# Optimization experiments

Hardware: AMD Instinct MI355X
Metric: run time of the kernel (lower is better)

The kernel has to match this reference:

```python
import jax, jax.numpy as jnp
import numpy as np

K = 21                     # kernel_size
LAM = 128.0                # lam
SIGMA_SPACE = 32.0
SIGMA_LUMA = 8.0
H = 512
W = 512
HO = H - K + 1             # valid conv output height (492)
WO = W - K + 1
C = (K - 1) // 2           # center offset (10)
CTR = C * K + C            # center channel index in row-major K*K patches


def _diff_patches(x):
    """x: (H, W) float. Returns (K*K-1, HO, WO): center pixel minus each
    of the other K*K-1 window taps (== the sparse 2-tap conv in torch)."""
    p = jax.lax.conv_general_dilated_patches(
        x[None, None], (K, K), (1, 1), 'VALID')[0]      # (K*K, HO, WO)
    diffs = p[CTR][None] - p                             # center - neighbor
    return jnp.delete(diffs, CTR, axis=0)                # drop all-zero center chan


def _make_w_ij(ref_hwc):
    """Bilateral affinity weights, per the torch __init__."""
    pos_x = jnp.broadcast_to(jnp.arange(W, dtype=jnp.float32)[None, :], (H, W))
    pos_y = jnp.broadcast_to(jnp.arange(H, dtype=jnp.float32)[:, None], (H, W))
    dx = _diff_patches(pos_x)
    dy = _diff_patches(pos_y)
    log_w = -(dx * dx + dy * dy) / (2.0 * SIGMA_SPACE ** 2)
    for c in range(ref_hwc.shape[-1]):                   # fixed 3 channels
        dr = _diff_patches(ref_hwc[:, :, c])
        log_w = log_w - dr * dr / (2.0 * SIGMA_LUMA ** 2)
    return jnp.exp(log_w)                                # (K*K-1, HO, WO)


def setup_inputs() -> dict:
    key = jax.random.key(0)
    k1, k2, k3 = jax.random.split(key, 3)
    output = jax.random.uniform(k1, (H, W), dtype=jnp.float32)   # logits/255
    target = jax.random.uniform(k2, (H, W), dtype=jnp.float32)   # target/255
    ref = jax.random.uniform(k3, (H, W, 3), dtype=jnp.float32) * 255.0
    w_ij = _make_w_ij(ref)
    bias = jnp.zeros((K * K - 1,), dtype=jnp.float32)   # torch conv bias (zeroed)
    return {"output": output, "target": target, "w_ij": w_ij, "bias": bias}


def reference(output, target, w_ij, bias):
    d = _diff_patches(output) + bias[:, None, None]      # (K*K-1, HO, WO)
    smooth = (H * W) * LAM * jnp.mean(w_ij * d * d)
    fidelity = jnp.mean((output - target) ** 2)
    return smooth + fidelity
```

## Files before the change

### kernel.cpp

```cpp
#include <hip/hip_runtime.h>

constexpr int Kk   = 21;
constexpr int Hh   = 512, Ww = 512;
constexpr int HO   = 492, WO = 492;
constexpr int Cc   = 10;
constexpr int CTRi = 220;
constexpr int NCH  = 440;
constexpr int ROW4 = WO / 4;
constexpr int N4S  = NCH * HO * ROW4;
constexpr int N4F  = Hh * Ww / 4;

typedef float floatx4 __attribute__((ext_vector_type(4)));

#define TPB  256
#define NB_S 1024
#define NB_F 64

__device__ __forceinline__ float block_reduce_256(float v) {
    #pragma unroll
    for (int off = 32; off; off >>= 1) v += __shfl_down(v, off, 64);
    __shared__ float smem[TPB / 64];
    const int lane = threadIdx.x & 63;
    const int wid  = threadIdx.x >> 6;
    if (lane == 0) smem[wid] = v;
    __syncthreads();
    float r = 0.f;
    if (threadIdx.x == 0) {
        #pragma unroll
        for (int k = 0; k < TPB / 64; ++k) r += smem[k];
    }
    return r;
}

__global__ __launch_bounds__(TPB) void smooth_partial_kernel(
        const float* __restrict__ outp,
        const float* __restrict__ w,
        const float* __restrict__ bias,
        float* __restrict__ partial)
{
    float acc = 0.f;
    const int stride = gridDim.x * blockDim.x;
    for (int q = blockIdx.x * blockDim.x + threadIdx.x; q < N4S; q += stride) {
        const int r  = q / ROW4;
        const int j  = (q - r * ROW4) * 4;
        const int n  = r / HO;
        const int i  = r - n * HO;
        const int kk = n + (n >= CTRi ? 1 : 0);
        const int ki = kk / Kk;
        const int kj = kk - ki * Kk;

        const floatx4 w4 = __builtin_nontemporal_load(((const floatx4*)w) + q);

        const float* crow = outp + (i + Cc) * Ww + (Cc + j);
        const float* nrow = outp + (i + ki) * Ww + (kj + j);
        const float  b    = bias[n];

        const float d0 = crow[0] - nrow[0] + b;
        const float d1 = crow[1] - nrow[1] + b;
        const float d2 = crow[2] - nrow[2] + b;
        const float d3 = crow[3] - nrow[3] + b;

        acc += w4.x * d0 * d0 + w4.y * d1 * d1 + w4.z * d2 * d2 + w4.w * d3 * d3;
    }
    const float bsum = block_reduce_256(acc);
    if (threadIdx.x == 0) partial[blockIdx.x] = bsum;
}

__global__ __launch_bounds__(TPB) void fid_partial_kernel(
        const float* __restrict__ outp,
        const float* __restrict__ targ,
        float* __restrict__ partial)
{
    float acc = 0.f;
    const int stride = gridDim.x * blockDim.x;
    for (int q = blockIdx.x * blockDim.x + threadIdx.x; q < N4F; q += stride) {
        const floatx4 a = ((const floatx4*)outp)[q];
        const floatx4 t = ((const floatx4*)targ)[q];
        const float d0 = a.x - t.x, d1 = a.y - t.y, d2 = a.z - t.z, d3 = a.w - t.w;
        acc += d0 * d0 + d1 * d1 + d2 * d2 + d3 * d3;
    }
    const float bsum = block_reduce_256(acc);
    if (threadIdx.x == 0) partial[blockIdx.x] = bsum;
}

__global__ __launch_bounds__(64) void finalize_kernel(
        const float* __restrict__ ps,
        const float* __restrict__ pf,
        float* __restrict__ out)
{
    const int t = threadIdx.x;
    float s = 0.f;
    for (int i = t; i < NB_S; i += 64) s += ps[i];
    float f = pf[t];
    #pragma unroll
    for (int off = 32; off; off >>= 1) {
        s += __shfl_down(s, off, 64);
        f += __shfl_down(f, off, 64);
    }
    if (t == 0) {
        const float SCALE_S = (float)((512.0 * 512.0 * 128.0) / (440.0 * 492.0 * 492.0));
        const float SCALE_F = 1.0f / (512.0f * 512.0f);
        out[0] = s * SCALE_S + f * SCALE_F;
    }
}

extern "C" void kernel_launch(void* const* d_in, const int* in_sizes, int n_in,
                              void* d_out, int out_size, void* d_ws, size_t ws_size,
                              hipStream_t stream) {
    const float* outp = (const float*)d_in[0];
    const float* targ = (const float*)d_in[1];
    const float* w    = (const float*)d_in[2];
    const float* bias = (const float*)d_in[3];

    float* ps = (float*)d_ws;
    float* pf = ps + NB_S;

    smooth_partial_kernel<<<NB_S, TPB, 0, stream>>>(outp, w, bias, ps);
    fid_partial_kernel<<<NB_F, TPB, 0, stream>>>(outp, targ, pf);
    finalize_kernel<<<1, 64, 0, stream>>>(ps, pf, (float*)d_out);
}
```

Baseline: 559.2 us.

## Fuse fidelity into smooth kernel with row-block and channel-split tiling

```diff
diff --git a/kernel.cpp b/kernel.cpp
--- a/kernel.cpp
+++ b/kernel.cpp
@@ -7,14 +7,20 @@
 constexpr int CTRi = 220;
 constexpr int NCH  = 440;
 constexpr int ROW4 = WO / 4;
-constexpr int N4S  = NCH * HO * ROW4;
 constexpr int N4F  = Hh * Ww / 4;
+
+constexpr int RSPLIT = HO / 2;
+constexpr int CSPLIT = 8;
+constexpr int NPB    = NCH / CSPLIT;
+constexpr int NBLK   = RSPLIT * CSPLIT;
+
+constexpr float SCALE_S  = (float)((512.0 * 512.0 * 128.0) / (440.0 * 492.0 * 492.0));
+constexpr float FID_RATIO = (float)((1.0 / (512.0 * 512.0)) /
+                                    ((512.0 * 512.0 * 128.0) / (440.0 * 492.0 * 492.0)));
 
 typedef float floatx4 __attribute__((ext_vector_type(4)));
 
-#define TPB  256
-#define NB_S 1024
-#define NB_F 64
+#define TPB 256
 
 __device__ __forceinline__ float block_reduce_256(float v) {
     #pragma unroll
@@ -32,76 +38,79 @@
     return r;
 }
 
-__global__ __launch_bounds__(TPB) void smooth_partial_kernel(
+__global__ __launch_bounds__(TPB) void main_kernel(
         const float* __restrict__ outp,
+        const float* __restrict__ targ,
         const float* __restrict__ w,
         const float* __restrict__ bias,
         float* __restrict__ partial)
 {
+    const int t = threadIdx.x;
     float acc = 0.f;
-    const int stride = gridDim.x * blockDim.x;
-    for (int q = blockIdx.x * blockDim.x + threadIdx.x; q < N4S; q += stride) {
-        const int r  = q / ROW4;
-        const int j  = (q - r * ROW4) * 4;
-        const int n  = r / HO;
-        const int i  = r - n * HO;
-        const int kk = n + (n >= CTRi ? 1 : 0);
-        const int ki = kk / Kk;
-        const int kj = kk - ki * Kk;
 
-        const floatx4 w4 = __builtin_nontemporal_load(((const floatx4*)w) + q);
+    {
+        const int fq = blockIdx.x * TPB + t;
+        if (fq < N4F) {
+            const floatx4 a  = ((const floatx4*)outp)[fq];
+            const floatx4 tg = ((const floatx4*)targ)[fq];
+            const float d0 = a.x - tg.x, d1 = a.y - tg.y,
+                        d2 = a.z - tg.z, d3 = a.w - tg.w;
+            acc = (d0 * d0 + d1 * d1 + d2 * d2 + d3 * d3) * FID_RATIO;
+        }
+    }
+
+    const int rowblk = blockIdx.x % RSPLIT;
+    const int csplit = blockIdx.x / RSPLIT;
+    const int n0     = csplit * NPB;
+
+    if (t < 2 * ROW4) {
+        const int di = (t >= ROW4) ? 1 : 0;
+        const int j4 = t - di * ROW4;
+        const int i  = rowblk * 2 + di;
+        const int j  = 4 * j4;
 
         const float* crow = outp + (i + Cc) * Ww + (Cc + j);
-        const float* nrow = outp + (i + ki) * Ww + (kj + j);
-        const float  b    = bias[n];
+        const float c0 = crow[0], c1 = crow[1], c2 = crow[2], c3 = crow[3];
 
-        const float d0 = crow[0] - nrow[0] + b;
-        const float d1 = crow[1] - nrow[1] + b;
-        const float d2 = crow[2] - nrow[2] + b;
-        const float d3 = crow[3] - nrow[3] + b;
+        const float* obase = outp + i * Ww + j;
+        const floatx4* wp  = (const floatx4*)w + ((long)(n0 * HO + i) * ROW4 + j4);
 
-        acc += w4.x * d0 * d0 + w4.y * d1 * d1 + w4.z * d2 * d2 + w4.w * d3 * d3;
+        float a0 = 0.f, a1 = 0.f, a2 = 0.f, a3 = 0.f;
+        #pragma unroll 5
+        for (int n = n0; n < n0 + NPB; ++n, wp += HO * ROW4) {
+            const int kk = n + (n >= CTRi ? 1 : 0);
+            const int ki = kk / Kk;
+            const int kj = kk - ki * Kk;
+
+            const floatx4 w4 = __builtin_nontemporal_load(wp);
+            const float   b  = bias[n];
+            const float*  nr = obase + ki * Ww + kj;
+
+            const float d0 = c0 - nr[0] + b;
+            const float d1 = c1 - nr[1] + b;
+            const float d2 = c2 - nr[2] + b;
+            const float d3 = c3 - nr[3] + b;
+
+            a0 += w4.x * d0 * d0;
+            a1 += w4.y * d1 * d1;
+            a2 += w4.z * d2 * d2;
+            a3 += w4.w * d3 * d3;
+        }
+        acc += (a0 + a1) + (a2 + a3);
     }
+
     const float bsum = block_reduce_256(acc);
-    if (threadIdx.x == 0) partial[blockIdx.x] = bsum;
+    if (t == 0) partial[blockIdx.x] = bsum;
 }
 
-__global__ __launch_bounds__(TPB) void fid_partial_kernel(
-        const float* __restrict__ outp,
-        const float* __restrict__ targ,
-        float* __restrict__ partial)
-{
-    float acc = 0.f;
-    const int stride = gridDim.x * blockDim.x;
-    for (int q = blockIdx.x * blockDim.x + threadIdx.x; q < N4F; q += stride) {
-        const floatx4 a = ((const floatx4*)outp)[q];
-        const floatx4 t = ((const floatx4*)targ)[q];
-        const float d0 = a.x - t.x, d1 = a.y - t.y, d2 = a.z - t.z, d3 = a.w - t.w;
-        acc += d0 * d0 + d1 * d1 + d2 * d2 + d3 * d3;
-    }
-    const float bsum = block_reduce_256(acc);
-    if (threadIdx.x == 0) partial[blockIdx.x] = bsum;
-}
-
-__global__ __launch_bounds__(64) void finalize_kernel(
-        const float* __restrict__ ps,
-        const float* __restrict__ pf,
+__global__ __launch_bounds__(TPB) void finalize_kernel(
+        const float* __restrict__ partial,
         float* __restrict__ out)
 {
-    const int t = threadIdx.x;
-    float s = 0.f;
-    for (int i = t; i < NB_S; i += 64) s += ps[i];
-    float f = pf[t];
-    #pragma unroll
-    for (int off = 32; off; off >>= 1) {
-        s += __shfl_down(s, off, 64);
-        f += __shfl_down(f, off, 64);
-    }
-    if (t == 0) {
-        const float SCALE_S = (float)((512.0 * 512.0 * 128.0) / (440.0 * 492.0 * 492.0));
-        const float SCALE_F = 1.0f / (512.0f * 512.0f);
-        out[0] = s * SCALE_S + f * SCALE_F;
-    }
+    float v = 0.f;
+    for (int idx = threadIdx.x; idx < NBLK; idx += TPB) v += partial[idx];
+    const float s = block_reduce_256(v);
+    if (threadIdx.x == 0) out[0] = s * SCALE_S;
 }
 
 extern "C" void kernel_launch(void* const* d_in, const int* in_sizes, int n_in,
@@ -112,10 +121,8 @@
     const float* w    = (const float*)d_in[2];
     const float* bias = (const float*)d_in[3];
 
-    float* ps = (float*)d_ws;
-    float* pf = ps + NB_S;
+    float* partial = (float*)d_ws;
 
-    smooth_partial_kernel<<<NB_S, TPB, 0, stream>>>(outp, w, bias, ps);
-    fid_partial_kernel<<<NB_F, TPB, 0, stream>>>(outp, targ, pf);
-    finalize_kernel<<<1, 64, 0, stream>>>(ps, pf, (float*)d_out);
+    main_kernel<<<NBLK, TPB, 0, stream>>>(outp, targ, w, bias, partial);
+    finalize_kernel<<<1, TPB, 0, stream>>>(partial, (float*)d_out);
 }
```

Result: faster. 525.0 us (-6.1%).
